# Performance work log

Hardware: AMD Instinct MI355X
Metric: run time of the kernel (lower is better)

## Reference

```python
import jax, jax.numpy as jnp
import numpy as np


def setup_inputs() -> dict:
    key = jax.random.key(0)
    k1, k2, k3 = jax.random.split(key, 3)
    B, q_len, c_len, D = 8, 512, 4096, 256  # D = 2*hidden_size
    q = jax.random.normal(k1, (B, q_len, D), dtype=jnp.float32)
    c = jax.random.normal(k2, (B, c_len, D), dtype=jnp.float32)
    # wsim: nn.Linear(3*D, 1, bias=False) -> weight vector of length 3*D
    w = jax.random.normal(k3, (3 * D,), dtype=jnp.float32) * (1.0 / np.sqrt(3 * D))
    return {"q": q, "c": c, "w": w}


def reference(q, c, w):
    # q: [B, q_len, D], c: [B, c_len, D], w: [3D] (concatenated [w_q, w_c, w_m])
    D = q.shape[-1]
    w_q, w_c, w_m = w[:D], w[D:2 * D], w[2 * D:]
    # S[b,i,j] = w . [q_j, c_i, q_j*c_i]  (decomposed trilinear score, no 6H blowup)
    S = (c @ w_c)[:, :, None] + (q @ w_q)[:, None, :] \
        + jnp.einsum('bid,bjd->bij', c * w_m, q)  # [B, c_len, q_len]
    # context2query: softmax over query dim, then attend over q
    context2query = jnp.einsum('bij,bjd->bid', jax.nn.softmax(S, axis=-1), q)
    # query2context: softmax over c of max-over-q scores, attend over c, broadcast to c_len
    b_attn = jax.nn.softmax(jnp.max(S, axis=2), axis=-1)  # [B, c_len]
    query2context = jnp.einsum('bi,bid->bd', b_attn, c)[:, None, :]  # [B, 1, D]
    query2context = jnp.broadcast_to(query2context, c.shape)  # repeat over c_len
    return jnp.concatenate(
        [c, context2query, c * context2query, c * query2context], axis=2
    )  # [B, c_len, 4D]
```

## Files before the change

kernel.cpp:

```cpp
#include <hip/hip_runtime.h>

#define BB 8
#define CL 4096
#define QL 512
#define DD 256

typedef unsigned short u16;
typedef unsigned char u8;
typedef long long i64;
typedef float f32x4 __attribute__((ext_vector_type(4)));
typedef short s16x8 __attribute__((ext_vector_type(8)));

static __device__ __forceinline__ u16 f2bf(float x) {
  unsigned int u = __float_as_uint(x);
  u += 0x7FFFu + ((u >> 16) & 1u);
  return (u16)(u >> 16);
}
static __device__ __forceinline__ float bf2f(u16 h) {
  return __uint_as_float(((unsigned int)h) << 16);
}

__global__ __launch_bounds__(256) void prep_q_k(
    const float* __restrict__ q, const float* __restrict__ w,
    u16* __restrict__ qbf, u8* __restrict__ qt8, float* __restrict__ qw_g)
{
  __shared__ u16 qs[8][256];
  __shared__ float red[8][32];
  int blk = blockIdx.x;
  int b = blk & 7;
  int j0 = (blk >> 3) * 8;
  int t = threadIdx.x;
  int r = t >> 5;
  int cs = (t & 31) * 8;

  const float* qrow = q + ((size_t)(b * QL + j0 + r)) * DD + cs;
  float4 v0 = *(const float4*)(qrow);
  float4 v1 = *(const float4*)(qrow + 4);
  float4 w0 = *(const float4*)(w + cs);
  float4 w1 = *(const float4*)(w + cs + 4);
  float pw = v0.x*w0.x + v0.y*w0.y + v0.z*w0.z + v0.w*w0.w
           + v1.x*w1.x + v1.y*w1.y + v1.z*w1.z + v1.w*w1.w;

  union { u16 u[8]; uint4 v; } pk;
  pk.u[0]=f2bf(v0.x); pk.u[1]=f2bf(v0.y); pk.u[2]=f2bf(v0.z); pk.u[3]=f2bf(v0.w);
  pk.u[4]=f2bf(v1.x); pk.u[5]=f2bf(v1.y); pk.u[6]=f2bf(v1.z); pk.u[7]=f2bf(v1.w);

  *(uint4*)(qbf + ((size_t)(b * QL + j0 + r)) * DD + cs) = pk.v;
  *(uint4*)(&qs[r][cs]) = pk.v;
  red[r][t & 31] = pw;
  __syncthreads();

  if (t < 8) {
    float s = 0.f;
    #pragma unroll
    for (int k = 0; k < 32; ++k) s += red[t][k];
    qw_g[b * QL + j0 + t] = s;
  }

  int d = t;
  float f[8];
  #pragma unroll
  for (int jj = 0; jj < 8; ++jj) f[jj] = bf2f(qs[jj][d]);
  unsigned int lo = __builtin_amdgcn_cvt_pk_fp8_f32(f[0], f[1], 0u, false);
  lo = __builtin_amdgcn_cvt_pk_fp8_f32(f[2], f[3], lo, true);
  unsigned int hi = __builtin_amdgcn_cvt_pk_fp8_f32(f[4], f[5], 0u, false);
  hi = __builtin_amdgcn_cvt_pk_fp8_f32(f[6], f[7], hi, true);
  *(unsigned int*)(qt8 + ((size_t)(b * DD + d)) * QL + j0) = lo;
  *(unsigned int*)(qt8 + ((size_t)(b * DD + d)) * QL + j0 + 4) = hi;
}

__global__ __launch_bounds__(512, 4) void attn_main_k(
    const float* __restrict__ c, const float* __restrict__ w,
    const u16* __restrict__ qbf, const u8* __restrict__ qt8,
    const float* __restrict__ qw_g,
    float* __restrict__ pm_g, float* __restrict__ z_g,
    float* __restrict__ part_g, float* __restrict__ out)
{
  __shared__ u8 pool8[64 * 512];
  __shared__ float qw_s[QL];
  __shared__ float cw_s[64];
  __shared__ float red_m[64][8];
  __shared__ float red_z[64][8];

  u16* cm = (u16*)pool8;

  int t = threadIdx.x;
  int blk = blockIdx.x;
  int b = blk & 7;
  int tile = blk >> 3;
  int it0 = tile * 64;

  int wv = t >> 6;
  int ln = t & 63;
  int lr = ln & 15;
  int lg = ln >> 4;
  int jc = wv * 64;
  int aswz = (lr & 7) << 3;

  {
    int r = t >> 3;
    int cg = (t & 7) * 32;
    int swz = (r & 7) << 3;
    const float* crow = c + ((size_t)(b * CL + it0 + r)) * DD + cg;
    float* outrow = out + ((size_t)(b * CL + it0 + r)) * (4 * DD) + cg;
    float pcw = 0.f;
    #pragma unroll
    for (int u = 0; u < 32; u += 4) {
      f32x4 cv  = *(const f32x4*)(crow + u);
      f32x4 wcv = *(const f32x4*)(w + DD + cg + u);
      f32x4 wmv = *(const f32x4*)(w + 2 * DD + cg + u);
      *(f32x4*)(outrow + u) = cv;
      pcw += cv[0]*wcv[0] + cv[1]*wcv[1] + cv[2]*wcv[2] + cv[3]*wcv[3];
      ushort4 hv;
      hv.x = f2bf(cv[0] * wmv[0]); hv.y = f2bf(cv[1] * wmv[1]);
      hv.z = f2bf(cv[2] * wmv[2]); hv.w = f2bf(cv[3] * wmv[3]);
      *(ushort4*)(&cm[r * 256 + ((cg + u) ^ swz)]) = hv;
    }
    pcw += __shfl_xor(pcw, 1);
    pcw += __shfl_xor(pcw, 2);
    pcw += __shfl_xor(pcw, 4);
    if ((t & 7) == 0) cw_s[r] = pcw;
    qw_s[t] = qw_g[b * QL + t];
  }
  __syncthreads();

  f32x4 acc[4][4];
  #pragma unroll
  for (int m = 0; m < 4; ++m)
    #pragma unroll
    for (int n = 0; n < 4; ++n) acc[m][n] = (f32x4){0.f, 0.f, 0.f, 0.f};

  const u16* qb = qbf + (size_t)b * QL * DD + (size_t)(jc + lr) * DD + lg * 8;
  #pragma unroll
  for (int kk = 0; kk < 8; ++kk) {
    s16x8 a[4];
    #pragma unroll
    for (int m = 0; m < 4; ++m)
      a[m] = *(const s16x8*)(&cm[(m * 16 + lr) * 256 + ((kk * 32 + lg * 8) ^ aswz)]);
    #pragma unroll
    for (int nh = 0; nh < 4; nh += 2) {
      s16x8 bq0 = *(const s16x8*)(qb + (size_t)(nh * 16) * DD + kk * 32);
      s16x8 bq1 = *(const s16x8*)(qb + (size_t)((nh + 1) * 16) * DD + kk * 32);
      #pragma unroll
      for (int m = 0; m < 4; ++m) {
        acc[m][nh]     = __builtin_amdgcn_mfma_f32_16x16x32_bf16(bq0, a[m], acc[m][nh], 0, 0, 0);
        acc[m][nh + 1] = __builtin_amdgcn_mfma_f32_16x16x32_bf16(bq1, a[m], acc[m][nh + 1], 0, 0, 0);
      }
    }
  }

  #pragma unroll
  for (int m = 0; m < 4; ++m) {
    float mx = -1e30f;
    float s = 0.f;
    #pragma unroll
    for (int n = 0; n < 4; ++n) {
      f32x4 qq = *(const f32x4*)(&qw_s[jc + n * 16 + lg * 4]);
      #pragma unroll
      for (int rr = 0; rr < 4; ++rr) {
        float sv = acc[m][n][rr] + qq[rr];
        mx = fmaxf(mx, sv);
        float e = __expf(sv);
        acc[m][n][rr] = e;
        s += e;
      }
    }
    mx = fmaxf(mx, __shfl_xor(mx, 16));
    mx = fmaxf(mx, __shfl_xor(mx, 32));
    s += __shfl_xor(s, 16);
    s += __shfl_xor(s, 32);
    if (lg == 0) { red_m[m * 16 + lr][wv] = mx; red_z[m * 16 + lr][wv] = s; }
  }
  __syncthreads();

  #pragma unroll
  for (int m = 0; m < 4; ++m) {
    int row = m * 16 + lr;
    size_t rb = (size_t)row * 512;
    #pragma unroll
    for (int n = 0; n < 4; ++n) {
      unsigned int p4 = __builtin_amdgcn_cvt_pk_fp8_f32(acc[m][n][0], acc[m][n][1], 0u, false);
      p4 = __builtin_amdgcn_cvt_pk_fp8_f32(acc[m][n][2], acc[m][n][3], p4, true);
      *(unsigned int*)(pool8 + rb + (((unsigned)(jc + n * 16 + lg * 4)) ^ aswz)) = p4;
    }
  }
  __syncthreads();

  f32x4 o2[4][2];
  #pragma unroll
  for (int m = 0; m < 4; ++m)
    #pragma unroll
    for (int n = 0; n < 2; ++n) o2[m][n] = (f32x4){0.f, 0.f, 0.f, 0.f};

  int dc = wv * 32;
  const u8* qt = qt8 + (size_t)b * DD * QL + (size_t)(dc + lr) * QL + lg * 8;
  #pragma unroll
  for (int kk = 0; kk < 16; ++kk) {
    i64 bv0 = *(const i64*)(qt + kk * 32);
    i64 bv1 = *(const i64*)(qt + (size_t)16 * QL + kk * 32);
    i64 pa[4];
    #pragma unroll
    for (int m = 0; m < 4; ++m)
      pa[m] = *(const i64*)(pool8 + (size_t)(m * 16 + lr) * 512 + (((unsigned)(kk * 32 + lg * 8)) ^ aswz));
    #pragma unroll
    for (int m = 0; m < 4; ++m) {
      o2[m][0] = __builtin_amdgcn_mfma_f32_16x16x32_fp8_fp8(bv0, pa[m], o2[m][0], 0, 0, 0);
      o2[m][1] = __builtin_amdgcn_mfma_f32_16x16x32_fp8_fp8(bv1, pa[m], o2[m][1], 0, 0, 0);
    }
  }

  float invz[4], wgt[4], mt[4];
  float pmx = -1e30f;
  #pragma unroll
  for (int m = 0; m < 4; ++m) {
    int i = m * 16 + lr;
    float4 m0 = *(const float4*)(&red_m[i][0]);
    float4 m1 = *(const float4*)(&red_m[i][4]);
    mt[m] = cw_s[i] + fmaxf(fmaxf(fmaxf(m0.x, m0.y), fmaxf(m0.z, m0.w)),
                            fmaxf(fmaxf(m1.x, m1.y), fmaxf(m1.z, m1.w)));
    pmx = fmaxf(pmx, mt[m]);
    float4 z0 = *(const float4*)(&red_z[i][0]);
    float4 z1 = *(const float4*)(&red_z[i][4]);
    invz[m] = 1.0f / (z0.x + z0.y + z0.z + z0.w + z1.x + z1.y + z1.z + z1.w);
  }
  pmx = fmaxf(pmx, __shfl_xor(pmx, 1));
  pmx = fmaxf(pmx, __shfl_xor(pmx, 2));
  pmx = fmaxf(pmx, __shfl_xor(pmx, 4));
  pmx = fmaxf(pmx, __shfl_xor(pmx, 8));
  float zs = 0.f;
  #pragma unroll
  for (int m = 0; m < 4; ++m) { wgt[m] = __expf(mt[m] - pmx); zs += wgt[m]; }
  zs += __shfl_xor(zs, 1);
  zs += __shfl_xor(zs, 2);
  zs += __shfl_xor(zs, 4);
  zs += __shfl_xor(zs, 8);
  if (t == 0) { pm_g[b * 64 + tile] = pmx; z_g[b * 64 + tile] = zs; }

  const float* cb = c + ((size_t)(b * CL + it0)) * DD;
  float* ob = out + ((size_t)(b * CL + it0)) * (4 * DD);
  #pragma unroll
  for (int n = 0; n < 2; ++n) {
    int d4 = dc + n * 16 + lg * 4;
    f32x4 psum = (f32x4){0.f, 0.f, 0.f, 0.f};
    #pragma unroll
    for (int m = 0; m < 4; ++m) {
      int i = m * 16 + lr;
      f32x4 cv = *(const f32x4*)(cb + (size_t)i * DD + d4);
      f32x4 c2q = o2[m][n] * invz[m];
      float* orow = ob + (size_t)i * (4 * DD);
      *(f32x4*)(orow + DD + d4) = c2q;
      *(f32x4*)(orow + 2 * DD + d4) = cv * c2q;
      psum += wgt[m] * cv;
    }
    #pragma unroll
    for (int j = 0; j < 4; ++j) {
      psum[j] += __shfl_xor(psum[j], 1);
      psum[j] += __shfl_xor(psum[j], 2);
      psum[j] += __shfl_xor(psum[j], 4);
      psum[j] += __shfl_xor(psum[j], 8);
    }
    if (lr == 0)
      *(f32x4*)(part_g + ((size_t)(b * 64 + tile)) * DD + d4) = psum;
  }
}

__global__ __launch_bounds__(256) void q2c_seg3_k(
    const float* __restrict__ c,
    const float* __restrict__ pm_g, const float* __restrict__ z_g,
    const float* __restrict__ part_g, float* __restrict__ out)
{
  __shared__ float wk[64];
  int blk = blockIdx.x;
  int b = blk & 7;
  int chunk = blk >> 3;
  int t = threadIdx.x;

  if (t < 64) {
    float p = pm_g[b * 64 + t];
    float m = p;
    #pragma unroll
    for (int o = 1; o < 64; o <<= 1) m = fmaxf(m, __shfl_xor(m, o));
    float ew = __expf(p - m);
    float zi = ew * z_g[b * 64 + t];
    float s = zi;
    #pragma unroll
    for (int o = 1; o < 64; o <<= 1) s += __shfl_xor(s, o);
    wk[t] = ew / s;
  }
  __syncthreads();

  int c4 = (t & 63) * 4;
  f32x4 g = (f32x4){0.f, 0.f, 0.f, 0.f};
  #pragma unroll 8
  for (int k = 0; k < 64; ++k)
    g += wk[k] * *(const f32x4*)(part_g + ((size_t)(b * 64 + k)) * DD + c4);

  int r0 = chunk * 128 + (t >> 6);
  for (int it = 0; it < 32; ++it) {
    int row = r0 + it * 4;
    f32x4 cv = *(const f32x4*)(c + ((size_t)(b * CL + row)) * DD + c4);
    *(f32x4*)(out + ((size_t)(b * CL + row)) * (4 * DD) + 3 * DD + c4) = cv * g;
  }
}

extern "C" void kernel_launch(void* const* d_in, const int* in_sizes, int n_in,
                              void* d_out, int out_size, void* d_ws, size_t ws_size,
                              hipStream_t stream) {
  const float* q = (const float*)d_in[0];
  const float* c = (const float*)d_in[1];
  const float* w = (const float*)d_in[2];
  float* out = (float*)d_out;
  char* ws = (char*)d_ws;

  u16*   qbf  = (u16*)(ws);
  u8*    qt8  = (u8*)(ws + 2097152);
  float* qw   = (float*)(ws + 3145728);
  float* pm   = (float*)(ws + 3162112);
  float* zb   = (float*)(ws + 3164160);
  float* part = (float*)(ws + 3166208);

  prep_q_k<<<512, 256, 0, stream>>>(q, w, qbf, qt8, qw);
  attn_main_k<<<512, 512, 0, stream>>>(c, w, qbf, qt8, qw, pm, zb, part, out);
  q2c_seg3_k<<<256, 256, 0, stream>>>(c, pm, zb, part, out);
}
```

Before: 89.65 us.

## Keep c*w_m fragments in registers and stream q panels through double-buffered LDS

The first GEMM is restructured. Each wave now holds its 16-row slice of c*w_m as bf16 MFMA operands in registers, while q is staged through LDS in 32-row panels with double buffering and register prefetch, instead of every wave reading q directly from global memory. Exp, max and sum are computed per panel and written straight into the fp8 P buffer. The copy of c into the first output segment moves into the epilogue, which removes the separate c staging pass. The cost is a __syncthreads in each of the 16 panel iterations, only 16 MFMAs per panel per wave, and higher register pressure from holding the operand fragments.

```diff
diff --git a/kernel.cpp b/kernel.cpp
--- a/kernel.cpp
+++ b/kernel.cpp
@@ -8,8 +8,10 @@
 typedef unsigned short u16;
 typedef unsigned char u8;
 typedef long long i64;
+typedef unsigned int u32;
 typedef float f32x4 __attribute__((ext_vector_type(4)));
 typedef short s16x8 __attribute__((ext_vector_type(8)));
+typedef unsigned int u32x4 __attribute__((ext_vector_type(4)));
 
 static __device__ __forceinline__ u16 f2bf(float x) {
   unsigned int u = __float_as_uint(x);
@@ -76,13 +78,12 @@
     float* __restrict__ pm_g, float* __restrict__ z_g,
     float* __restrict__ part_g, float* __restrict__ out)
 {
-  __shared__ u8 pool8[64 * 512];
+  __shared__ u16 qpan[2][32 * 256];
+  __shared__ u8  P[64 * 512];
   __shared__ float qw_s[QL];
   __shared__ float cw_s[64];
-  __shared__ float red_m[64][8];
-  __shared__ float red_z[64][8];
-
-  u16* cm = (u16*)pool8;
+  __shared__ float red_m[64][2];
+  __shared__ float red_z[64][2];
 
   int t = threadIdx.x;
   int blk = blockIdx.x;
@@ -94,96 +95,87 @@
   int ln = t & 63;
   int lr = ln & 15;
   int lg = ln >> 4;
-  int jc = wv * 64;
-  int aswz = (lr & 7) << 3;
-
+  int iw = wv >> 1;
+  int jw = wv & 1;
+
+  int clm = ln & 31;
+  int jlA = 2 * wv + (ln >> 5);
+  int jlB = jlA + 16;
+  int wA = jlA * 256 + ((clm ^ (jlA & 7)) * 8);
+  int wB = jlB * 256 + ((clm ^ (jlB & 7)) * 8);
+  const u16* qsrc = qbf + (size_t)b * QL * DD;
+
+  u32x4 sA = *(const u32x4*)(qsrc + (size_t)jlA * 256 + clm * 8);
+  u32x4 sB = *(const u32x4*)(qsrc + (size_t)jlB * 256 + clm * 8);
+
+  s16x8 cmf[8];
+  float pcw = 0.f;
   {
-    int r = t >> 3;
-    int cg = (t & 7) * 32;
-    int swz = (r & 7) << 3;
-    const float* crow = c + ((size_t)(b * CL + it0 + r)) * DD + cg;
-    float* outrow = out + ((size_t)(b * CL + it0 + r)) * (4 * DD) + cg;
-    float pcw = 0.f;
-    #pragma unroll
-    for (int u = 0; u < 32; u += 4) {
-      f32x4 cv  = *(const f32x4*)(crow + u);
-      f32x4 wcv = *(const f32x4*)(w + DD + cg + u);
-      f32x4 wmv = *(const f32x4*)(w + 2 * DD + cg + u);
-      *(f32x4*)(outrow + u) = cv;
-      pcw += cv[0]*wcv[0] + cv[1]*wcv[1] + cv[2]*wcv[2] + cv[3]*wcv[3];
-      ushort4 hv;
-      hv.x = f2bf(cv[0] * wmv[0]); hv.y = f2bf(cv[1] * wmv[1]);
-      hv.z = f2bf(cv[2] * wmv[2]); hv.w = f2bf(cv[3] * wmv[3]);
-      *(ushort4*)(&cm[r * 256 + ((cg + u) ^ swz)]) = hv;
-    }
-    pcw += __shfl_xor(pcw, 1);
-    pcw += __shfl_xor(pcw, 2);
-    pcw += __shfl_xor(pcw, 4);
-    if ((t & 7) == 0) cw_s[r] = pcw;
-    qw_s[t] = qw_g[b * QL + t];
-  }
-  __syncthreads();
-
-  f32x4 acc[4][4];
-  #pragma unroll
-  for (int m = 0; m < 4; ++m)
-    #pragma unroll
-    for (int n = 0; n < 4; ++n) acc[m][n] = (f32x4){0.f, 0.f, 0.f, 0.f};
-
-  const u16* qb = qbf + (size_t)b * QL * DD + (size_t)(jc + lr) * DD + lg * 8;
-  #pragma unroll
-  for (int kk = 0; kk < 8; ++kk) {
-    s16x8 a[4];
-    #pragma unroll
-    for (int m = 0; m < 4; ++m)
-      a[m] = *(const s16x8*)(&cm[(m * 16 + lr) * 256 + ((kk * 32 + lg * 8) ^ aswz)]);
-    #pragma unroll
-    for (int nh = 0; nh < 4; nh += 2) {
-      s16x8 bq0 = *(const s16x8*)(qb + (size_t)(nh * 16) * DD + kk * 32);
-      s16x8 bq1 = *(const s16x8*)(qb + (size_t)((nh + 1) * 16) * DD + kk * 32);
-      #pragma unroll
-      for (int m = 0; m < 4; ++m) {
-        acc[m][nh]     = __builtin_amdgcn_mfma_f32_16x16x32_bf16(bq0, a[m], acc[m][nh], 0, 0, 0);
-        acc[m][nh + 1] = __builtin_amdgcn_mfma_f32_16x16x32_bf16(bq1, a[m], acc[m][nh + 1], 0, 0, 0);
-      }
-    }
-  }
-
-  #pragma unroll
-  for (int m = 0; m < 4; ++m) {
-    float mx = -1e30f;
-    float s = 0.f;
-    #pragma unroll
-    for (int n = 0; n < 4; ++n) {
-      f32x4 qq = *(const f32x4*)(&qw_s[jc + n * 16 + lg * 4]);
-      #pragma unroll
-      for (int rr = 0; rr < 4; ++rr) {
-        float sv = acc[m][n][rr] + qq[rr];
-        mx = fmaxf(mx, sv);
-        float e = __expf(sv);
-        acc[m][n][rr] = e;
-        s += e;
-      }
-    }
-    mx = fmaxf(mx, __shfl_xor(mx, 16));
-    mx = fmaxf(mx, __shfl_xor(mx, 32));
-    s += __shfl_xor(s, 16);
-    s += __shfl_xor(s, 32);
-    if (lg == 0) { red_m[m * 16 + lr][wv] = mx; red_z[m * 16 + lr][wv] = s; }
-  }
-  __syncthreads();
-
-  #pragma unroll
-  for (int m = 0; m < 4; ++m) {
-    int row = m * 16 + lr;
-    size_t rb = (size_t)row * 512;
-    #pragma unroll
-    for (int n = 0; n < 4; ++n) {
-      unsigned int p4 = __builtin_amdgcn_cvt_pk_fp8_f32(acc[m][n][0], acc[m][n][1], 0u, false);
-      p4 = __builtin_amdgcn_cvt_pk_fp8_f32(acc[m][n][2], acc[m][n][3], p4, true);
-      *(unsigned int*)(pool8 + rb + (((unsigned)(jc + n * 16 + lg * 4)) ^ aswz)) = p4;
-    }
-  }
+    const float* crow = c + (size_t)(b * CL + it0 + iw * 16 + lr) * DD + lg * 8;
+    const float* wc = w + DD + lg * 8;
+    const float* wm = w + 2 * DD + lg * 8;
+    #pragma unroll
+    for (int kk = 0; kk < 8; ++kk) {
+      f32x4 c0  = *(const f32x4*)(crow + kk * 32);
+      f32x4 c1  = *(const f32x4*)(crow + kk * 32 + 4);
+      f32x4 wc0 = *(const f32x4*)(wc + kk * 32);
+      f32x4 wc1 = *(const f32x4*)(wc + kk * 32 + 4);
+      f32x4 wm0 = *(const f32x4*)(wm + kk * 32);
+      f32x4 wm1 = *(const f32x4*)(wm + kk * 32 + 4);
+      pcw += c0[0]*wc0[0] + c0[1]*wc0[1] + c0[2]*wc0[2] + c0[3]*wc0[3]
+           + c1[0]*wc1[0] + c1[1]*wc1[1] + c1[2]*wc1[2] + c1[3]*wc1[3];
+      union { u16 u[8]; s16x8 v; } pk;
+      pk.u[0] = f2bf(c0[0]*wm0[0]); pk.u[1] = f2bf(c0[1]*wm0[1]);
+      pk.u[2] = f2bf(c0[2]*wm0[2]); pk.u[3] = f2bf(c0[3]*wm0[3]);
+      pk.u[4] = f2bf(c1[0]*wm1[0]); pk.u[5] = f2bf(c1[1]*wm1[1]);
+      pk.u[6] = f2bf(c1[2]*wm1[2]); pk.u[7] = f2bf(c1[3]*wm1[3]);
+      cmf[kk] = pk.v;
+    }
+  }
+  pcw += __shfl_xor(pcw, 16);
+  pcw += __shfl_xor(pcw, 32);
+  if (jw == 0 && lg == 0) cw_s[iw * 16 + lr] = pcw;
+  qw_s[t] = qw_g[b * QL + t];
+
+  float zacc = 0.f, macc = -1e30f;
+  int jrow = jw * 16 + lr;
+  int aoff = jrow * 256;
+  int aswz = (jrow & 7) << 3;
+  int pi = iw * 16 + lr;
+  int piswz = (pi & 7) << 3;
+
+  for (int p = 0; p < 16; ++p) {
+    u16* qb = &qpan[p & 1][0];
+    *(u32x4*)(qb + wA) = sA;
+    *(u32x4*)(qb + wB) = sB;
+    __syncthreads();
+    if (p < 15) {
+      sA = *(const u32x4*)(qsrc + (size_t)((p + 1) * 32 + jlA) * 256 + clm * 8);
+      sB = *(const u32x4*)(qsrc + (size_t)((p + 1) * 32 + jlB) * 256 + clm * 8);
+    }
+    f32x4 acc = (f32x4){0.f, 0.f, 0.f, 0.f};
+    #pragma unroll
+    for (int kk = 0; kk < 8; ++kk) {
+      s16x8 aq = *(const s16x8*)(qb + aoff + ((kk * 32 + lg * 8) ^ aswz));
+      acc = __builtin_amdgcn_mfma_f32_16x16x32_bf16(aq, cmf[kk], acc, 0, 0, 0);
+    }
+    f32x4 qq = *(const f32x4*)(&qw_s[p * 32 + jw * 16 + lg * 4]);
+    float s0 = acc[0] + qq[0], s1 = acc[1] + qq[1];
+    float s2 = acc[2] + qq[2], s3 = acc[3] + qq[3];
+    macc = fmaxf(macc, fmaxf(fmaxf(s0, s1), fmaxf(s2, s3)));
+    float e0 = __expf(s0), e1 = __expf(s1), e2 = __expf(s2), e3 = __expf(s3);
+    zacc += (e0 + e1) + (e2 + e3);
+    u32 p4 = __builtin_amdgcn_cvt_pk_fp8_f32(e0, e1, 0u, false);
+    p4 = __builtin_amdgcn_cvt_pk_fp8_f32(e2, e3, p4, true);
+    int pj = p * 32 + jw * 16 + lg * 4;
+    *(u32*)(P + pi * 512 + (pj ^ piswz)) = p4;
+  }
+
+  zacc += __shfl_xor(zacc, 16);
+  zacc += __shfl_xor(zacc, 32);
+  macc = fmaxf(macc, __shfl_xor(macc, 16));
+  macc = fmaxf(macc, __shfl_xor(macc, 32));
+  if (lg == 0) { red_z[pi][jw] = zacc; red_m[pi][jw] = macc; }
   __syncthreads();
 
   f32x4 o2[4][2];
@@ -200,8 +192,10 @@
     i64 bv1 = *(const i64*)(qt + (size_t)16 * QL + kk * 32);
     i64 pa[4];
     #pragma unroll
-    for (int m = 0; m < 4; ++m)
-      pa[m] = *(const i64*)(pool8 + (size_t)(m * 16 + lr) * 512 + (((unsigned)(kk * 32 + lg * 8)) ^ aswz));
+    for (int m = 0; m < 4; ++m) {
+      int pr = m * 16 + lr;
+      pa[m] = *(const i64*)(P + pr * 512 + ((kk * 32 + lg * 8) ^ ((pr & 7) << 3)));
+    }
     #pragma unroll
     for (int m = 0; m < 4; ++m) {
       o2[m][0] = __builtin_amdgcn_mfma_f32_16x16x32_fp8_fp8(bv0, pa[m], o2[m][0], 0, 0, 0);
@@ -214,14 +208,9 @@
   #pragma unroll
   for (int m = 0; m < 4; ++m) {
     int i = m * 16 + lr;
-    float4 m0 = *(const float4*)(&red_m[i][0]);
-    float4 m1 = *(const float4*)(&red_m[i][4]);
-    mt[m] = cw_s[i] + fmaxf(fmaxf(fmaxf(m0.x, m0.y), fmaxf(m0.z, m0.w)),
-                            fmaxf(fmaxf(m1.x, m1.y), fmaxf(m1.z, m1.w)));
+    mt[m] = cw_s[i] + fmaxf(red_m[i][0], red_m[i][1]);
     pmx = fmaxf(pmx, mt[m]);
-    float4 z0 = *(const float4*)(&red_z[i][0]);
-    float4 z1 = *(const float4*)(&red_z[i][4]);
-    invz[m] = 1.0f / (z0.x + z0.y + z0.z + z0.w + z1.x + z1.y + z1.z + z1.w);
+    invz[m] = 1.0f / (red_z[i][0] + red_z[i][1]);
   }
   pmx = fmaxf(pmx, __shfl_xor(pmx, 1));
   pmx = fmaxf(pmx, __shfl_xor(pmx, 2));
@@ -248,6 +237,7 @@
       f32x4 cv = *(const f32x4*)(cb + (size_t)i * DD + d4);
       f32x4 c2q = o2[m][n] * invz[m];
       float* orow = ob + (size_t)i * (4 * DD);
+      *(f32x4*)(orow + d4) = cv;
       *(f32x4*)(orow + DD + d4) = c2q;
       *(f32x4*)(orow + 2 * DD + d4) = cv * c2q;
       psum += wgt[m] * cv;
```

After: 94.58 us. 1.06x slower.

## Stage context2query through LDS for row-contiguous output stores and block reductions

Applied to the files above, without the earlier changes.

The MFMA result tile is normalized, rounded to bf16 and written into swizzled shared memory. It is then read back row-wise so each thread writes 32 contiguous floats per output row, where before the stores followed the scattered MFMA fragment layout. The query2context max and sum and the weighted c partial sums become block-wide reductions through shuffles and a shared buffer. The aim is better store coalescing, at the cost of extra barriers, LDS traffic, and bf16 rounding of the context2query output, which loses precision.

```diff
diff --git a/kernel.cpp b/kernel.cpp
--- a/kernel.cpp
+++ b/kernel.cpp
@@ -8,6 +8,7 @@
 typedef unsigned short u16;
 typedef unsigned char u8;
 typedef long long i64;
+typedef unsigned int u32;
 typedef float f32x4 __attribute__((ext_vector_type(4)));
 typedef short s16x8 __attribute__((ext_vector_type(8)));
 
@@ -81,6 +82,8 @@
   __shared__ float cw_s[64];
   __shared__ float red_m[64][8];
   __shared__ float red_z[64][8];
+  __shared__ float red2[8][256];
+  __shared__ float smx_s;
 
   u16* cm = (u16*)pool8;
 
@@ -209,58 +212,95 @@
     }
   }
 
-  float invz[4], wgt[4], mt[4];
-  float pmx = -1e30f;
+  float invz[4];
   #pragma unroll
   for (int m = 0; m < 4; ++m) {
     int i = m * 16 + lr;
-    float4 m0 = *(const float4*)(&red_m[i][0]);
-    float4 m1 = *(const float4*)(&red_m[i][4]);
-    mt[m] = cw_s[i] + fmaxf(fmaxf(fmaxf(m0.x, m0.y), fmaxf(m0.z, m0.w)),
-                            fmaxf(fmaxf(m1.x, m1.y), fmaxf(m1.z, m1.w)));
-    pmx = fmaxf(pmx, mt[m]);
     float4 z0 = *(const float4*)(&red_z[i][0]);
     float4 z1 = *(const float4*)(&red_z[i][4]);
     invz[m] = 1.0f / (z0.x + z0.y + z0.z + z0.w + z1.x + z1.y + z1.z + z1.w);
   }
-  pmx = fmaxf(pmx, __shfl_xor(pmx, 1));
-  pmx = fmaxf(pmx, __shfl_xor(pmx, 2));
-  pmx = fmaxf(pmx, __shfl_xor(pmx, 4));
-  pmx = fmaxf(pmx, __shfl_xor(pmx, 8));
-  float zs = 0.f;
-  #pragma unroll
-  for (int m = 0; m < 4; ++m) { wgt[m] = __expf(mt[m] - pmx); zs += wgt[m]; }
-  zs += __shfl_xor(zs, 1);
-  zs += __shfl_xor(zs, 2);
-  zs += __shfl_xor(zs, 4);
-  zs += __shfl_xor(zs, 8);
-  if (t == 0) { pm_g[b * 64 + tile] = pmx; z_g[b * 64 + tile] = zs; }
-
-  const float* cb = c + ((size_t)(b * CL + it0)) * DD;
-  float* ob = out + ((size_t)(b * CL + it0)) * (4 * DD);
-  #pragma unroll
-  for (int n = 0; n < 2; ++n) {
-    int d4 = dc + n * 16 + lg * 4;
-    f32x4 psum = (f32x4){0.f, 0.f, 0.f, 0.f};
-    #pragma unroll
-    for (int m = 0; m < 4; ++m) {
-      int i = m * 16 + lr;
-      f32x4 cv = *(const f32x4*)(cb + (size_t)i * DD + d4);
-      f32x4 c2q = o2[m][n] * invz[m];
-      float* orow = ob + (size_t)i * (4 * DD);
-      *(f32x4*)(orow + DD + d4) = c2q;
-      *(f32x4*)(orow + 2 * DD + d4) = cv * c2q;
-      psum += wgt[m] * cv;
-    }
-    #pragma unroll
-    for (int j = 0; j < 4; ++j) {
-      psum[j] += __shfl_xor(psum[j], 1);
-      psum[j] += __shfl_xor(psum[j], 2);
-      psum[j] += __shfl_xor(psum[j], 4);
-      psum[j] += __shfl_xor(psum[j], 8);
-    }
-    if (lr == 0)
-      *(f32x4*)(part_g + ((size_t)(b * 64 + tile)) * DD + d4) = psum;
+  __syncthreads();
+
+  u16* c2qs = (u16*)pool8;
+  #pragma unroll
+  for (int m = 0; m < 4; ++m) {
+    int row = m * 16 + lr;
+    int rswz = (row & 7) << 3;
+    #pragma unroll
+    for (int n = 0; n < 2; ++n) {
+      f32x4 v = o2[m][n] * invz[m];
+      ushort4 hv;
+      hv.x = f2bf(v[0]); hv.y = f2bf(v[1]); hv.z = f2bf(v[2]); hv.w = f2bf(v[3]);
+      int col = dc + n * 16 + lg * 4;
+      *(ushort4*)(&c2qs[row * 256 + (col ^ rswz)]) = hv;
+    }
+  }
+
+  if (wv == 0) {
+    int row = ln;
+    float4 m0 = *(const float4*)(&red_m[row][0]);
+    float4 m1 = *(const float4*)(&red_m[row][4]);
+    float mt = cw_s[row] + fmaxf(fmaxf(fmaxf(m0.x, m0.y), fmaxf(m0.z, m0.w)),
+                                 fmaxf(fmaxf(m1.x, m1.y), fmaxf(m1.z, m1.w)));
+    float pmx = mt;
+    #pragma unroll
+    for (int o = 1; o < 64; o <<= 1) pmx = fmaxf(pmx, __shfl_xor(pmx, o));
+    float wg = __expf(mt - pmx);
+    float zs = wg;
+    #pragma unroll
+    for (int o = 1; o < 64; o <<= 1) zs += __shfl_xor(zs, o);
+    if (ln == 0) {
+      smx_s = pmx;
+      pm_g[b * 64 + tile] = pmx;
+      z_g[b * 64 + tile] = zs;
+    }
+  }
+  __syncthreads();
+
+  {
+    int r = t >> 3;
+    int cc = (t & 7) * 32;
+    int rswz = (r & 7) << 3;
+    float4 m0 = *(const float4*)(&red_m[r][0]);
+    float4 m1 = *(const float4*)(&red_m[r][4]);
+    float mt = cw_s[r] + fmaxf(fmaxf(fmaxf(m0.x, m0.y), fmaxf(m0.z, m0.w)),
+                               fmaxf(fmaxf(m1.x, m1.y), fmaxf(m1.z, m1.w)));
+    float wg = __expf(mt - smx_s);
+    const float* crow = c + ((size_t)(b * CL + it0 + r)) * DD + cc;
+    float* orow = out + ((size_t)(b * CL + it0 + r)) * (4 * DD);
+    f32x4 pp[8];
+    #pragma unroll
+    for (int u = 0; u < 8; ++u) {
+      f32x4 cv = *(const f32x4*)(crow + u * 4);
+      ushort4 h = *(const ushort4*)(&c2qs[r * 256 + ((cc + u * 4) ^ rswz)]);
+      f32x4 cq;
+      cq[0] = bf2f(h.x); cq[1] = bf2f(h.y); cq[2] = bf2f(h.z); cq[3] = bf2f(h.w);
+      *(f32x4*)(orow + DD + cc + u * 4) = cq;
+      *(f32x4*)(orow + 2 * DD + cc + u * 4) = cv * cq;
+      pp[u] = wg * cv;
+    }
+    #pragma unroll
+    for (int u = 0; u < 8; ++u)
+      #pragma unroll
+      for (int j = 0; j < 4; ++j) {
+        pp[u][j] += __shfl_xor(pp[u][j], 8);
+        pp[u][j] += __shfl_xor(pp[u][j], 16);
+        pp[u][j] += __shfl_xor(pp[u][j], 32);
+      }
+    if ((ln >> 3) == 0) {
+      #pragma unroll
+      for (int u = 0; u < 8; ++u)
+        *(f32x4*)(&red2[wv][cc + u * 4]) = pp[u];
+    }
+  }
+  __syncthreads();
+
+  if (t < 256) {
+    float s = 0.f;
+    #pragma unroll
+    for (int wvi = 0; wvi < 8; ++wvi) s += red2[wvi][t];
+    part_g[((size_t)(b * 64 + tile)) * DD + t] = s;
   }
 }
 
```

Measured after the change: 109.6 us. +22.2%, slower.

## Split fused attention kernel into separate score and PV GEMM kernels via global fp8 P

Applied to the files above, without the earlier changes.

The single attention kernel that computed scores, softmax and P·Q in shared memory is split into two kernels. The first writes fp8 exp-scores plus per-row max and inverse sum to workspace. The second runs the P·Q fp8 MFMA over 32-row tiles on 1024 blocks and does the c2q outputs and partial q2c sums. Copying c into the first output segment moves to the final q2c kernel, which now reduces over 128 partial tiles. The aim is to shorten critical paths and raise parallelism, at the cost of a 16 MB round trip through global memory for P and one extra launch.

```diff
diff --git a/kernel.cpp b/kernel.cpp
--- a/kernel.cpp
+++ b/kernel.cpp
@@ -8,6 +8,7 @@
 typedef unsigned short u16;
 typedef unsigned char u8;
 typedef long long i64;
+typedef unsigned int u32;
 typedef float f32x4 __attribute__((ext_vector_type(4)));
 typedef short s16x8 __attribute__((ext_vector_type(8)));
 
@@ -69,20 +70,17 @@
   *(unsigned int*)(qt8 + ((size_t)(b * DD + d)) * QL + j0 + 4) = hi;
 }
 
-__global__ __launch_bounds__(512, 4) void attn_main_k(
+__global__ __launch_bounds__(512, 4) void gemm1_k(
     const float* __restrict__ c, const float* __restrict__ w,
-    const u16* __restrict__ qbf, const u8* __restrict__ qt8,
-    const float* __restrict__ qw_g,
-    float* __restrict__ pm_g, float* __restrict__ z_g,
-    float* __restrict__ part_g, float* __restrict__ out)
+    const u16* __restrict__ qbf, const float* __restrict__ qw_g,
+    u8* __restrict__ pg, float* __restrict__ mrow_g,
+    float* __restrict__ zinv_g)
 {
-  __shared__ u8 pool8[64 * 512];
+  __shared__ u16 cm[64 * 256];
   __shared__ float qw_s[QL];
   __shared__ float cw_s[64];
   __shared__ float red_m[64][8];
   __shared__ float red_z[64][8];
-
-  u16* cm = (u16*)pool8;
 
   int t = threadIdx.x;
   int blk = blockIdx.x;
@@ -102,14 +100,12 @@
     int cg = (t & 7) * 32;
     int swz = (r & 7) << 3;
     const float* crow = c + ((size_t)(b * CL + it0 + r)) * DD + cg;
-    float* outrow = out + ((size_t)(b * CL + it0 + r)) * (4 * DD) + cg;
     float pcw = 0.f;
     #pragma unroll
     for (int u = 0; u < 32; u += 4) {
       f32x4 cv  = *(const f32x4*)(crow + u);
       f32x4 wcv = *(const f32x4*)(w + DD + cg + u);
       f32x4 wmv = *(const f32x4*)(w + 2 * DD + cg + u);
-      *(f32x4*)(outrow + u) = cv;
       pcw += cv[0]*wcv[0] + cv[1]*wcv[1] + cv[2]*wcv[2] + cv[3]*wcv[3];
       ushort4 hv;
       hv.x = f2bf(cv[0] * wmv[0]); hv.y = f2bf(cv[1] * wmv[1]);
@@ -149,104 +145,127 @@
     }
   }
 
+  u8* pb = pg + ((size_t)(b * CL + it0)) * 512;
   #pragma unroll
   for (int m = 0; m < 4; ++m) {
+    int row = m * 16 + lr;
     float mx = -1e30f;
     float s = 0.f;
     #pragma unroll
     for (int n = 0; n < 4; ++n) {
       f32x4 qq = *(const f32x4*)(&qw_s[jc + n * 16 + lg * 4]);
-      #pragma unroll
-      for (int rr = 0; rr < 4; ++rr) {
-        float sv = acc[m][n][rr] + qq[rr];
-        mx = fmaxf(mx, sv);
-        float e = __expf(sv);
-        acc[m][n][rr] = e;
-        s += e;
+      float e0, e1, e2, e3;
+      {
+        float s0 = acc[m][n][0] + qq[0];
+        float s1 = acc[m][n][1] + qq[1];
+        float s2 = acc[m][n][2] + qq[2];
+        float s3 = acc[m][n][3] + qq[3];
+        mx = fmaxf(mx, fmaxf(fmaxf(s0, s1), fmaxf(s2, s3)));
+        e0 = __expf(s0); e1 = __expf(s1); e2 = __expf(s2); e3 = __expf(s3);
+        s += (e0 + e1) + (e2 + e3);
       }
+      u32 p4 = __builtin_amdgcn_cvt_pk_fp8_f32(e0, e1, 0u, false);
+      p4 = __builtin_amdgcn_cvt_pk_fp8_f32(e2, e3, p4, true);
+      *(u32*)(pb + (size_t)row * 512 + jc + n * 16 + lg * 4) = p4;
     }
     mx = fmaxf(mx, __shfl_xor(mx, 16));
     mx = fmaxf(mx, __shfl_xor(mx, 32));
     s += __shfl_xor(s, 16);
     s += __shfl_xor(s, 32);
-    if (lg == 0) { red_m[m * 16 + lr][wv] = mx; red_z[m * 16 + lr][wv] = s; }
-  }
-  __syncthreads();
-
-  #pragma unroll
-  for (int m = 0; m < 4; ++m) {
-    int row = m * 16 + lr;
-    size_t rb = (size_t)row * 512;
-    #pragma unroll
-    for (int n = 0; n < 4; ++n) {
-      unsigned int p4 = __builtin_amdgcn_cvt_pk_fp8_f32(acc[m][n][0], acc[m][n][1], 0u, false);
-      p4 = __builtin_amdgcn_cvt_pk_fp8_f32(acc[m][n][2], acc[m][n][3], p4, true);
-      *(unsigned int*)(pool8 + rb + (((unsigned)(jc + n * 16 + lg * 4)) ^ aswz)) = p4;
-    }
-  }
-  __syncthreads();
-
-  f32x4 o2[4][2];
-  #pragma unroll
-  for (int m = 0; m < 4; ++m)
-    #pragma unroll
-    for (int n = 0; n < 2; ++n) o2[m][n] = (f32x4){0.f, 0.f, 0.f, 0.f};
-
-  int dc = wv * 32;
+    if (lg == 0) { red_m[row][wv] = mx; red_z[row][wv] = s; }
+  }
+  __syncthreads();
+
+  if (wv == 0) {
+    int row = ln;
+    float4 m0 = *(const float4*)(&red_m[row][0]);
+    float4 m1 = *(const float4*)(&red_m[row][4]);
+    float mt = cw_s[row] + fmaxf(fmaxf(fmaxf(m0.x, m0.y), fmaxf(m0.z, m0.w)),
+                                 fmaxf(fmaxf(m1.x, m1.y), fmaxf(m1.z, m1.w)));
+    float4 z0 = *(const float4*)(&red_z[row][0]);
+    float4 z1 = *(const float4*)(&red_z[row][4]);
+    float z = z0.x + z0.y + z0.z + z0.w + z1.x + z1.y + z1.z + z1.w;
+    mrow_g[b * CL + it0 + row] = mt;
+    zinv_g[b * CL + it0 + row] = 1.0f / z;
+  }
+}
+
+__global__ __launch_bounds__(256, 4) void gemm2_k(
+    const float* __restrict__ c, const u8* __restrict__ qt8,
+    const u8* __restrict__ pg, const float* __restrict__ mrow_g,
+    const float* __restrict__ zinv_g,
+    float* __restrict__ pm_g, float* __restrict__ z_g,
+    float* __restrict__ part_g, float* __restrict__ out)
+{
+  int t = threadIdx.x;
+  int blk = blockIdx.x;
+  int b = blk & 7;
+  int ht = blk >> 3;
+  int it0 = ht * 32;
+
+  int wv = t >> 6;
+  int ln = t & 63;
+  int lr = ln & 15;
+  int lg = ln >> 4;
+  int dc = wv * 64;
+
+  f32x4 o2[2][4];
+  #pragma unroll
+  for (int m = 0; m < 2; ++m)
+    #pragma unroll
+    for (int n = 0; n < 4; ++n) o2[m][n] = (f32x4){0.f, 0.f, 0.f, 0.f};
+
   const u8* qt = qt8 + (size_t)b * DD * QL + (size_t)(dc + lr) * QL + lg * 8;
-  #pragma unroll
+  const u8* pb = pg + ((size_t)(b * CL + it0)) * 512 + lg * 8;
+  #pragma unroll 4
   for (int kk = 0; kk < 16; ++kk) {
-    i64 bv0 = *(const i64*)(qt + kk * 32);
-    i64 bv1 = *(const i64*)(qt + (size_t)16 * QL + kk * 32);
-    i64 pa[4];
-    #pragma unroll
-    for (int m = 0; m < 4; ++m)
-      pa[m] = *(const i64*)(pool8 + (size_t)(m * 16 + lr) * 512 + (((unsigned)(kk * 32 + lg * 8)) ^ aswz));
-    #pragma unroll
-    for (int m = 0; m < 4; ++m) {
-      o2[m][0] = __builtin_amdgcn_mfma_f32_16x16x32_fp8_fp8(bv0, pa[m], o2[m][0], 0, 0, 0);
-      o2[m][1] = __builtin_amdgcn_mfma_f32_16x16x32_fp8_fp8(bv1, pa[m], o2[m][1], 0, 0, 0);
-    }
-  }
-
-  float invz[4], wgt[4], mt[4];
-  float pmx = -1e30f;
-  #pragma unroll
-  for (int m = 0; m < 4; ++m) {
-    int i = m * 16 + lr;
-    float4 m0 = *(const float4*)(&red_m[i][0]);
-    float4 m1 = *(const float4*)(&red_m[i][4]);
-    mt[m] = cw_s[i] + fmaxf(fmaxf(fmaxf(m0.x, m0.y), fmaxf(m0.z, m0.w)),
-                            fmaxf(fmaxf(m1.x, m1.y), fmaxf(m1.z, m1.w)));
-    pmx = fmaxf(pmx, mt[m]);
-    float4 z0 = *(const float4*)(&red_z[i][0]);
-    float4 z1 = *(const float4*)(&red_z[i][4]);
-    invz[m] = 1.0f / (z0.x + z0.y + z0.z + z0.w + z1.x + z1.y + z1.z + z1.w);
-  }
+    i64 bv[4];
+    #pragma unroll
+    for (int n = 0; n < 4; ++n)
+      bv[n] = *(const i64*)(qt + (size_t)(n * 16) * QL + kk * 32);
+    i64 pa[2];
+    #pragma unroll
+    for (int m = 0; m < 2; ++m)
+      pa[m] = *(const i64*)(pb + (size_t)(m * 16 + lr) * 512 + kk * 32);
+    #pragma unroll
+    for (int m = 0; m < 2; ++m)
+      #pragma unroll
+      for (int n = 0; n < 4; ++n)
+        o2[m][n] = __builtin_amdgcn_mfma_f32_16x16x32_fp8_fp8(bv[n], pa[m], o2[m][n], 0, 0, 0);
+  }
+
+  float mr[2], zi[2], wgt[2];
+  #pragma unroll
+  for (int m = 0; m < 2; ++m) {
+    int i = it0 + m * 16 + lr;
+    mr[m] = mrow_g[b * CL + i];
+    zi[m] = zinv_g[b * CL + i];
+  }
+  float pmx = fmaxf(mr[0], mr[1]);
   pmx = fmaxf(pmx, __shfl_xor(pmx, 1));
   pmx = fmaxf(pmx, __shfl_xor(pmx, 2));
   pmx = fmaxf(pmx, __shfl_xor(pmx, 4));
   pmx = fmaxf(pmx, __shfl_xor(pmx, 8));
-  float zs = 0.f;
-  #pragma unroll
-  for (int m = 0; m < 4; ++m) { wgt[m] = __expf(mt[m] - pmx); zs += wgt[m]; }
+  wgt[0] = __expf(mr[0] - pmx);
+  wgt[1] = __expf(mr[1] - pmx);
+  float zs = wgt[0] + wgt[1];
   zs += __shfl_xor(zs, 1);
   zs += __shfl_xor(zs, 2);
   zs += __shfl_xor(zs, 4);
   zs += __shfl_xor(zs, 8);
-  if (t == 0) { pm_g[b * 64 + tile] = pmx; z_g[b * 64 + tile] = zs; }
+  if (t == 0) { pm_g[b * 128 + ht] = pmx; z_g[b * 128 + ht] = zs; }
 
   const float* cb = c + ((size_t)(b * CL + it0)) * DD;
   float* ob = out + ((size_t)(b * CL + it0)) * (4 * DD);
   #pragma unroll
-  for (int n = 0; n < 2; ++n) {
+  for (int n = 0; n < 4; ++n) {
     int d4 = dc + n * 16 + lg * 4;
     f32x4 psum = (f32x4){0.f, 0.f, 0.f, 0.f};
     #pragma unroll
-    for (int m = 0; m < 4; ++m) {
+    for (int m = 0; m < 2; ++m) {
       int i = m * 16 + lr;
       f32x4 cv = *(const f32x4*)(cb + (size_t)i * DD + d4);
-      f32x4 c2q = o2[m][n] * invz[m];
+      f32x4 c2q = o2[m][n] * zi[m];
       float* orow = ob + (size_t)i * (4 * DD);
       *(f32x4*)(orow + DD + d4) = c2q;
       *(f32x4*)(orow + 2 * DD + d4) = cv * c2q;
@@ -260,7 +279,7 @@
       psum[j] += __shfl_xor(psum[j], 8);
     }
     if (lr == 0)
-      *(f32x4*)(part_g + ((size_t)(b * 64 + tile)) * DD + d4) = psum;
+      *(f32x4*)(part_g + ((size_t)(b * 128 + ht)) * DD + d4) = psum;
   }
 }
 
@@ -269,37 +288,49 @@
     const float* __restrict__ pm_g, const float* __restrict__ z_g,
     const float* __restrict__ part_g, float* __restrict__ out)
 {
-  __shared__ float wk[64];
+  __shared__ float wk[128];
+  __shared__ float rm[2];
+  __shared__ float rz[2];
   int blk = blockIdx.x;
   int b = blk & 7;
   int chunk = blk >> 3;
   int t = threadIdx.x;
 
-  if (t < 64) {
-    float p = pm_g[b * 64 + t];
+  float p = (t < 128) ? pm_g[b * 128 + t] : -1e30f;
+  if (t < 128) {
     float m = p;
     #pragma unroll
     for (int o = 1; o < 64; o <<= 1) m = fmaxf(m, __shfl_xor(m, o));
-    float ew = __expf(p - m);
-    float zi = ew * z_g[b * 64 + t];
+    if ((t & 63) == 0) rm[t >> 6] = m;
+  }
+  __syncthreads();
+  float M = fmaxf(rm[0], rm[1]);
+  if (t < 128) {
+    float ew = __expf(p - M);
+    float zi = ew * z_g[b * 128 + t];
     float s = zi;
     #pragma unroll
     for (int o = 1; o < 64; o <<= 1) s += __shfl_xor(s, o);
-    wk[t] = ew / s;
-  }
-  __syncthreads();
+    if ((t & 63) == 0) rz[t >> 6] = s;
+    wk[t] = ew;
+  }
+  __syncthreads();
+  float Zinv = 1.0f / (rz[0] + rz[1]);
 
   int c4 = (t & 63) * 4;
   f32x4 g = (f32x4){0.f, 0.f, 0.f, 0.f};
   #pragma unroll 8
-  for (int k = 0; k < 64; ++k)
-    g += wk[k] * *(const f32x4*)(part_g + ((size_t)(b * 64 + k)) * DD + c4);
+  for (int k = 0; k < 128; ++k)
+    g += wk[k] * *(const f32x4*)(part_g + ((size_t)(b * 128 + k)) * DD + c4);
+  g *= Zinv;
 
   int r0 = chunk * 128 + (t >> 6);
   for (int it = 0; it < 32; ++it) {
     int row = r0 + it * 4;
     f32x4 cv = *(const f32x4*)(c + ((size_t)(b * CL + row)) * DD + c4);
-    *(f32x4*)(out + ((size_t)(b * CL + row)) * (4 * DD) + 3 * DD + c4) = cv * g;
+    float* orow = out + ((size_t)(b * CL + row)) * (4 * DD);
+    *(f32x4*)(orow + c4) = cv;
+    *(f32x4*)(orow + 3 * DD + c4) = cv * g;
   }
 }
 
@@ -315,11 +346,15 @@
   u16*   qbf  = (u16*)(ws);
   u8*    qt8  = (u8*)(ws + 2097152);
   float* qw   = (float*)(ws + 3145728);
-  float* pm   = (float*)(ws + 3162112);
-  float* zb   = (float*)(ws + 3164160);
-  float* part = (float*)(ws + 3166208);
+  float* mrow = (float*)(ws + 3162112);
+  float* zinv = (float*)(ws + 3293184);
+  float* pm   = (float*)(ws + 3424256);
+  float* zb   = (float*)(ws + 3428352);
+  float* part = (float*)(ws + 3432448);
+  u8*    pg   = (u8*)(ws + 4481024);
 
   prep_q_k<<<512, 256, 0, stream>>>(q, w, qbf, qt8, qw);
-  attn_main_k<<<512, 512, 0, stream>>>(c, w, qbf, qt8, qw, pm, zb, part, out);
+  gemm1_k<<<512, 512, 0, stream>>>(c, w, qbf, qw, pg, mrow, zinv);
+  gemm2_k<<<1024, 256, 0, stream>>>(c, qt8, pg, mrow, zinv, pm, zb, part, out);
   q2c_seg3_k<<<256, 256, 0, stream>>>(c, pm, zb, part, out);
 }
```

New measurement: 120.4 us. +34.3%, slower.
